# Kernel tuning notes

Hardware: AMD Instinct MI355X
Metric: run time of the kernel (lower is better)

Reference implementation:

```python
import jax, jax.numpy as jnp
import numpy as np

N_NUM = 100        # numerical columns
N_CAT = 100        # categorical columns
CAT_COUNT = 100    # categories per categorical column
N_COND = 128
EPS = 1e-5         # torch GroupNorm default eps


def setup_inputs() -> dict:
    key = jax.random.key(0)
    ks = jax.random.split(key, 8)
    B = 4096
    return {
        "x_num": jax.random.normal(ks[0], (B, N_NUM), dtype=jnp.float32),
        "x_cat": jax.random.randint(ks[1], (B, N_CAT), 0, CAT_COUNT),
        "W_num": jax.random.normal(ks[2], (N_NUM, N_COND), dtype=jnp.float32),
        "b_num": jax.random.normal(ks[3], (N_NUM, N_COND), dtype=jnp.float32),
        "emb_table": jax.random.normal(ks[4], (N_CAT * CAT_COUNT, N_COND), dtype=jnp.float32),
        "gn_w": jnp.ones((N_CAT, N_COND), dtype=jnp.float32),
        "gn_b": jnp.zeros((N_CAT, N_COND), dtype=jnp.float32),
        "W_cat": jax.random.normal(ks[5], (N_CAT, N_COND, N_COND), dtype=jnp.float32) / np.sqrt(N_COND).astype(np.float32),
        "b_cat": jax.random.normal(ks[6], (N_CAT, N_COND), dtype=jnp.float32),
    }


def reference(x_num, x_cat, W_num, b_num, emb_table, gn_w, gn_b, W_cat, b_cat):
    # --- numerical branch: grouped 1x1 conv (Cin/g=1, Cout/g=n_cond) + sigmoid ---
    # (B, n_num, 1) * (n_num, n_cond) + bias -> (B, n_num, n_cond)
    num_emb = jax.nn.sigmoid(x_num[:, :, None] * W_num[None] + b_num[None])

    # --- categorical branch ---
    offsets = jnp.arange(N_CAT, dtype=x_cat.dtype) * CAT_COUNT  # cat_offset
    emb = emb_table[x_cat + offsets[None]]  # (B, n_cat, n_cond)

    # GroupNorm with n_cat groups over n_cat*n_cond channels (spatial dim = 1):
    # normalize each column's n_cond features per sample (biased variance).
    mean = jnp.mean(emb, axis=-1, keepdims=True)
    var = jnp.var(emb, axis=-1, keepdims=True)
    normed = (emb - mean) * jax.lax.rsqrt(var + EPS)
    normed = normed * gn_w[None] + gn_b[None]

    # grouped 1x1 conv, groups = n_cat: per-column n_cond x n_cond matmul
    cat_emb = jax.nn.sigmoid(jnp.einsum('bgi,gio->bgo', normed, W_cat) + b_cat[None])

    M = jnp.concatenate([num_emb, cat_emb], axis=1)  # (B, n_num+n_cat, n_cond)
    return jnp.transpose(M, (0, 2, 1))               # (B, n_cond, n_num+n_cat)
```

## Files before the change

### kernel.cpp

```cpp
#include <hip/hip_runtime.h>
#include <cstdint>

#define NNUM 100
#define NCAT 100
#define CATC 100
#define NCOND 128
#define GN_EPS 1e-5f

typedef __attribute__((ext_vector_type(8))) short bfrag8;
typedef __attribute__((ext_vector_type(4))) float accf4;

__device__ __forceinline__ float sigmoidf_(float x) { return 1.0f / (1.0f + __expf(-x)); }

__device__ __forceinline__ ushort f2bf(float f) {
    uint32_t u = __builtin_bit_cast(uint32_t, f);
    u += 0x7fffu + ((u >> 16) & 1u);
    return (ushort)(u >> 16);
}
__device__ __forceinline__ float bf2f(ushort h) {
    return __builtin_bit_cast(float, (uint32_t)h << 16);
}

__global__ __launch_bounds__(256)
void prep_wcat(const float* __restrict__ W_cat, ushort* __restrict__ Wf)
{
    const int g    = blockIdx.x;
    const int lane = threadIdx.x & 63;
    const int w    = threadIdx.x >> 6;
    const float* Wg = W_cat + ((size_t)g << 14);
    ushort* Wfg = Wf + ((size_t)g << 15);
    #pragma unroll
    for (int i = 0; i < 8; ++i) {
        int p  = w * 8 + i;
        int t  = p >> 2, kk = p & 3;
        int c  = t * 16 + (lane & 15);
        int kb = kk * 32 + ((lane >> 4) << 3);
        ushort hi[8], lo[8];
        #pragma unroll
        for (int j = 0; j < 8; ++j) {
            float v = Wg[(kb + j) * NCOND + c];
            ushort h = f2bf(v);
            hi[j] = h;
            lo[j] = f2bf(v - bf2f(h));
        }
        int off = ((t * 4 + kk) * 2) * 512 + lane * 8;
        *(bfrag8*)(Wfg + off)       = *(const bfrag8*)hi;
        *(bfrag8*)(Wfg + off + 512) = *(const bfrag8*)lo;
    }
}

template<int DIRECT>
__global__ __launch_bounds__(256, 2)
void cat_gemm_kernel(const int* __restrict__ x_cat,
                     const float* __restrict__ emb_table,
                     const float* __restrict__ gn_w,
                     const float* __restrict__ gn_b,
                     const ushort* __restrict__ Wf,
                     const float* __restrict__ b_cat,
                     float* __restrict__ dst)
{
    const int g    = blockIdx.y;
    const int b0   = blockIdx.x * 128;
    const int tid  = threadIdx.x;
    const int lane = tid & 63;
    const int w    = tid >> 6;

    __shared__ __align__(16) ushort Ahi[128 * 128];
    __shared__ __align__(16) ushort Alo[128 * 128];

    const int half = lane >> 5;
    const int l5   = lane & 31;
    float4 gwv = *(const float4*)(gn_w + g * NCOND + l5 * 4);
    float4 gbv = *(const float4*)(gn_b + g * NCOND + l5 * 4);

    #pragma unroll 4
    for (int it = 0; it < 16; ++it) {
        int m = w * 32 + it * 2 + half;
        int b = b0 + m;
        int idx = x_cat[(size_t)b * NCAT + g];
        const float4* row = (const float4*)(emb_table + ((size_t)(g * CATC + idx) << 7));
        float4 v = row[l5];
        float s  = v.x + v.y + v.z + v.w;
        float ss = v.x * v.x + v.y * v.y + v.z * v.z + v.w * v.w;
        #pragma unroll
        for (int off = 16; off > 0; off >>= 1) {
            s  += __shfl_xor(s,  off, 64);
            ss += __shfl_xor(ss, off, 64);
        }
        float mean = s * 0.0078125f;
        float var  = fmaf(-mean, mean, ss * 0.0078125f);
        float rs   = rsqrtf(var + GN_EPS);
        float n0 = fmaf((v.x - mean) * rs, gwv.x, gbv.x);
        float n1 = fmaf((v.y - mean) * rs, gwv.y, gbv.y);
        float n2 = fmaf((v.z - mean) * rs, gwv.z, gbv.z);
        float n3 = fmaf((v.w - mean) * rs, gwv.w, gbv.w);
        ushort h0 = f2bf(n0), h1 = f2bf(n1), h2 = f2bf(n2), h3 = f2bf(n3);
        uint2 hp = { (uint32_t)h0 | ((uint32_t)h1 << 16),
                     (uint32_t)h2 | ((uint32_t)h3 << 16) };
        uint2 lp = { (uint32_t)f2bf(n0 - bf2f(h0)) | ((uint32_t)f2bf(n1 - bf2f(h1)) << 16),
                     (uint32_t)f2bf(n2 - bf2f(h2)) | ((uint32_t)f2bf(n3 - bf2f(h3)) << 16) };
        int bo = m * 256 + ((l5 * 8) ^ ((m & 7) << 4));
        *(uint2*)((char*)Ahi + bo) = hp;
        *(uint2*)((char*)Alo + bo) = lp;
    }
    __syncthreads();

    accf4 acc[2][8];
    #pragma unroll
    for (int gi = 0; gi < 2; ++gi)
        #pragma unroll
        for (int t = 0; t < 8; ++t)
            acc[gi][t] = (accf4){0.f, 0.f, 0.f, 0.f};

    const ushort* Wfg = Wf + ((size_t)g << 15);
    const int row0 = w * 16 + (lane & 15);
    const int sw   = (lane & 7) << 4;

    #pragma unroll
    for (int kk = 0; kk < 4; ++kk) {
        int colb = kk * 64 + ((lane >> 4) << 4);
        int o0 = row0 * 256 + (colb ^ sw);
        int o1 = o0 + 64 * 256;
        bfrag8 ah0 = *(const bfrag8*)((const char*)Ahi + o0);
        bfrag8 al0 = *(const bfrag8*)((const char*)Alo + o0);
        bfrag8 ah1 = *(const bfrag8*)((const char*)Ahi + o1);
        bfrag8 al1 = *(const bfrag8*)((const char*)Alo + o1);
        const ushort* wbase = Wfg + kk * 1024 + lane * 8;
        #pragma unroll
        for (int t = 0; t < 8; ++t) {
            bfrag8 wh = *(const bfrag8*)(wbase + t * 4096);
            bfrag8 wl = *(const bfrag8*)(wbase + t * 4096 + 512);
            acc[0][t] = __builtin_amdgcn_mfma_f32_16x16x32_bf16(ah0, wh, acc[0][t], 0, 0, 0);
            acc[0][t] = __builtin_amdgcn_mfma_f32_16x16x32_bf16(ah0, wl, acc[0][t], 0, 0, 0);
            acc[0][t] = __builtin_amdgcn_mfma_f32_16x16x32_bf16(al0, wh, acc[0][t], 0, 0, 0);
            acc[1][t] = __builtin_amdgcn_mfma_f32_16x16x32_bf16(ah1, wh, acc[1][t], 0, 0, 0);
            acc[1][t] = __builtin_amdgcn_mfma_f32_16x16x32_bf16(ah1, wl, acc[1][t], 0, 0, 0);
            acc[1][t] = __builtin_amdgcn_mfma_f32_16x16x32_bf16(al1, wh, acc[1][t], 0, 0, 0);
        }
    }

    const float* bcg = b_cat + g * NCOND;
    const int colL = lane & 15;
    const int quad = lane >> 4;
    #pragma unroll
    for (int t = 0; t < 8; ++t) {
        int c = t * 16 + colL;
        float bc = bcg[c];
        #pragma unroll
        for (int gi = 0; gi < 2; ++gi) {
            int mbase = (w + gi * 4) * 16 + quad * 4;
            #pragma unroll
            for (int r = 0; r < 4; ++r) {
                int b = b0 + mbase + r;
                float v = sigmoidf_(acc[gi][t][r] + bc);
                if (DIRECT) {
                    dst[(size_t)b * (128 * 200) + (size_t)c * 200 + 100 + g] = v;
                } else {
                    dst[(size_t)b * (NCAT * NCOND) + g * NCOND + c] = v;
                }
            }
        }
    }
}

__global__ __launch_bounds__(256)
void transpose_wn(const float* __restrict__ W_num, const float* __restrict__ b_num,
                  float* __restrict__ Wt, float* __restrict__ Bt)
{
    int idx = blockIdx.x * 256 + threadIdx.x;
    if (idx < NCOND * NNUM) {
        int c = idx / NNUM, j = idx - c * NNUM;
        Wt[idx] = W_num[j * NCOND + c];
        Bt[idx] = b_num[j * NCOND + c];
    }
}

__global__ __launch_bounds__(256)
void finalize_kernel(const float* __restrict__ ws_cat,
                     const float* __restrict__ Wt,
                     const float* __restrict__ Bt,
                     const float* __restrict__ x_num,
                     float* __restrict__ out)
{
    const int b   = blockIdx.x;
    const int tid = threadIdx.x;
    __shared__ float T[NCAT * 129];
    __shared__ float xr[NNUM];

    if (tid < NNUM) xr[tid] = x_num[b * NNUM + tid];

    const float4* src = (const float4*)(ws_cat + (size_t)b * (NCAT * NCOND));
    #pragma unroll
    for (int it = 0; it < 13; ++it) {
        int i4 = it * 256 + tid;
        if (i4 < (NCAT * NCOND) / 4) {
            float4 v = src[i4];
            int base = i4 * 4;
            int gg = base >> 7;
            int cc = base & 127;
            float* d = &T[gg * 129 + cc];
            d[0] = v.x; d[1] = v.y; d[2] = v.z; d[3] = v.w;
        }
    }
    __syncthreads();

    float4* outb = (float4*)(out + (size_t)b * (NCOND * 200));
    const float4* Wt4 = (const float4*)Wt;
    const float4* Bt4 = (const float4*)Bt;
    #pragma unroll
    for (int it = 0; it < 25; ++it) {
        int o4 = it * 256 + tid;
        int c  = o4 / 50;
        int j4 = o4 - c * 50;
        float4 v;
        if (j4 < 25) {
            float4 wv = Wt4[c * 25 + j4];
            float4 bv = Bt4[c * 25 + j4];
            int j = j4 * 4;
            v.x = sigmoidf_(fmaf(xr[j],     wv.x, bv.x));
            v.y = sigmoidf_(fmaf(xr[j + 1], wv.y, bv.y));
            v.z = sigmoidf_(fmaf(xr[j + 2], wv.z, bv.z));
            v.w = sigmoidf_(fmaf(xr[j + 3], wv.w, bv.w));
        } else {
            int gg = (j4 - 25) * 4;
            v.x = T[(gg    ) * 129 + c];
            v.y = T[(gg + 1) * 129 + c];
            v.z = T[(gg + 2) * 129 + c];
            v.w = T[(gg + 3) * 129 + c];
        }
        outb[o4] = v;
    }
}

__global__ __launch_bounds__(256)
void num_direct(const float* __restrict__ x_num, const float* __restrict__ W_num,
                const float* __restrict__ b_num, float* __restrict__ out, int B)
{
    size_t i = (size_t)blockIdx.x * 256 + threadIdx.x;
    size_t total = (size_t)B * NCOND * NNUM;
    if (i >= total) return;
    int n = (int)(i % NNUM);
    size_t t = i / NNUM;
    int c = (int)(t % NCOND);
    int b = (int)(t / NCOND);
    float v = sigmoidf_(x_num[b * NNUM + n] * W_num[n * NCOND + c] + b_num[n * NCOND + c]);
    out[(size_t)b * (NCOND * 200) + (size_t)c * 200 + n] = v;
}

extern "C" void kernel_launch(void* const* d_in, const int* in_sizes, int n_in,
                              void* d_out, int out_size, void* d_ws, size_t ws_size,
                              hipStream_t stream)
{
    const float* x_num  = (const float*)d_in[0];
    const int*   x_cat  = (const int*)  d_in[1];
    const float* W_num  = (const float*)d_in[2];
    const float* b_num  = (const float*)d_in[3];
    const float* emb    = (const float*)d_in[4];
    const float* gn_w   = (const float*)d_in[5];
    const float* gn_b   = (const float*)d_in[6];
    const float* W_cat  = (const float*)d_in[7];
    const float* b_cat  = (const float*)d_in[8];
    float* out = (float*)d_out;

    const int B = in_sizes[0] / NNUM;
    const size_t cat_bytes = (size_t)B * NCAT * NCOND * sizeof(float);
    const size_t need = cat_bytes + 2 * (size_t)NCOND * NNUM * sizeof(float);

    dim3 gemm_grid(B / 128, NCAT);

    if (ws_size >= need) {
        float* ws_cat = (float*)d_ws;
        float* Wt = (float*)((char*)d_ws + cat_bytes);
        float* Bt = Wt + NCOND * NNUM;
        ushort* Wf = (ushort*)out;
        prep_wcat<<<NCAT, 256, 0, stream>>>(W_cat, Wf);
        transpose_wn<<<(NCOND * NNUM + 255) / 256, 256, 0, stream>>>(W_num, b_num, Wt, Bt);
        cat_gemm_kernel<0><<<gemm_grid, 256, 0, stream>>>(x_cat, emb, gn_w, gn_b, Wf, b_cat, ws_cat);
        finalize_kernel<<<B, 256, 0, stream>>>(ws_cat, Wt, Bt, x_num, out);
    } else {
        ushort* Wf = (ushort*)d_ws;
        prep_wcat<<<NCAT, 256, 0, stream>>>(W_cat, Wf);
        cat_gemm_kernel<1><<<gemm_grid, 256, 0, stream>>>(x_cat, emb, gn_w, gn_b, Wf, b_cat, out);
        size_t total = (size_t)B * NCOND * NNUM;
        num_direct<<<(total + 255) / 256, 256, 0, stream>>>(x_num, W_num, b_num, out, B);
    }
}
```

Before: 622.9 us.

## Drop block barrier in cat GEMM, shuffle indices, split finalize across channel halves

The categorical GEMM now loads each wave's category indices once and broadcasts them with shuffles, instead of one global load per row. Each wave now consumes only the A rows it wrote itself, so the block-wide barrier is replaced by an LDS wait. The finalize kernel is split into two blocks per sample, one per half of the channels, which halves its shared memory and raises occupancy. The packed weights move into the workspace when there is room for them. Together these aim to cut gather latency, barrier stalls and finalize occupancy limits, at the cost of depending on per-wave data ownership to stay correct.

```diff
diff --git a/kernel.cpp b/kernel.cpp
--- a/kernel.cpp
+++ b/kernel.cpp
@@ -73,11 +73,13 @@
     float4 gwv = *(const float4*)(gn_w + g * NCOND + l5 * 4);
     float4 gbv = *(const float4*)(gn_b + g * NCOND + l5 * 4);
 
-    #pragma unroll 4
+    int myidx = x_cat[(size_t)(b0 + w * 32 + (lane & 31)) * NCAT + g];
+
+    #pragma unroll 8
     for (int it = 0; it < 16; ++it) {
-        int m = w * 32 + it * 2 + half;
-        int b = b0 + m;
-        int idx = x_cat[(size_t)b * NCAT + g];
+        int r = it * 2 + half;
+        int m = w * 32 + r;
+        int idx = __shfl(myidx, r, 64);
         const float4* row = (const float4*)(emb_table + ((size_t)(g * CATC + idx) << 7));
         float4 v = row[l5];
         float s  = v.x + v.y + v.z + v.w;
@@ -103,7 +105,7 @@
         *(uint2*)((char*)Ahi + bo) = hp;
         *(uint2*)((char*)Alo + bo) = lp;
     }
-    __syncthreads();
+    asm volatile("s_waitcnt lgkmcnt(0)" ::: "memory");
 
     accf4 acc[2][8];
     #pragma unroll
@@ -113,14 +115,14 @@
             acc[gi][t] = (accf4){0.f, 0.f, 0.f, 0.f};
 
     const ushort* Wfg = Wf + ((size_t)g << 15);
-    const int row0 = w * 16 + (lane & 15);
+    const int row0 = w * 32 + (lane & 15);
     const int sw   = (lane & 7) << 4;
 
     #pragma unroll
     for (int kk = 0; kk < 4; ++kk) {
         int colb = kk * 64 + ((lane >> 4) << 4);
         int o0 = row0 * 256 + (colb ^ sw);
-        int o1 = o0 + 64 * 256;
+        int o1 = o0 + 16 * 256;
         bfrag8 ah0 = *(const bfrag8*)((const char*)Ahi + o0);
         bfrag8 al0 = *(const bfrag8*)((const char*)Alo + o0);
         bfrag8 ah1 = *(const bfrag8*)((const char*)Ahi + o1);
@@ -148,7 +150,7 @@
         float bc = bcg[c];
         #pragma unroll
         for (int gi = 0; gi < 2; ++gi) {
-            int mbase = (w + gi * 4) * 16 + quad * 4;
+            int mbase = (2 * w + gi) * 16 + quad * 4;
             #pragma unroll
             for (int r = 0; r < 4; ++r) {
                 int b = b0 + mbase + r;
@@ -183,52 +185,55 @@
                      float* __restrict__ out)
 {
     const int b   = blockIdx.x;
+    const int h   = blockIdx.y;
     const int tid = threadIdx.x;
-    __shared__ float T[NCAT * 129];
+    __shared__ float T[NCAT * 65];
     __shared__ float xr[NNUM];
 
     if (tid < NNUM) xr[tid] = x_num[b * NNUM + tid];
 
     const float4* src = (const float4*)(ws_cat + (size_t)b * (NCAT * NCOND));
     #pragma unroll
-    for (int it = 0; it < 13; ++it) {
+    for (int it = 0; it < 7; ++it) {
         int i4 = it * 256 + tid;
-        if (i4 < (NCAT * NCOND) / 4) {
-            float4 v = src[i4];
-            int base = i4 * 4;
-            int gg = base >> 7;
-            int cc = base & 127;
-            float* d = &T[gg * 129 + cc];
+        if (i4 < NCAT * 16) {
+            int gg  = i4 >> 4;
+            int cc4 = i4 & 15;
+            float4 v = src[gg * 32 + h * 16 + cc4];
+            float* d = &T[gg * 65 + cc4 * 4];
             d[0] = v.x; d[1] = v.y; d[2] = v.z; d[3] = v.w;
         }
     }
     __syncthreads();
 
-    float4* outb = (float4*)(out + (size_t)b * (NCOND * 200));
+    float4* outb = (float4*)(out + (size_t)b * (NCOND * 200)) + h * 3200;
     const float4* Wt4 = (const float4*)Wt;
     const float4* Bt4 = (const float4*)Bt;
     #pragma unroll
-    for (int it = 0; it < 25; ++it) {
+    for (int it = 0; it < 13; ++it) {
         int o4 = it * 256 + tid;
-        int c  = o4 / 50;
-        int j4 = o4 - c * 50;
-        float4 v;
-        if (j4 < 25) {
-            float4 wv = Wt4[c * 25 + j4];
-            float4 bv = Bt4[c * 25 + j4];
-            int j = j4 * 4;
-            v.x = sigmoidf_(fmaf(xr[j],     wv.x, bv.x));
-            v.y = sigmoidf_(fmaf(xr[j + 1], wv.y, bv.y));
-            v.z = sigmoidf_(fmaf(xr[j + 2], wv.z, bv.z));
-            v.w = sigmoidf_(fmaf(xr[j + 3], wv.w, bv.w));
-        } else {
-            int gg = (j4 - 25) * 4;
-            v.x = T[(gg    ) * 129 + c];
-            v.y = T[(gg + 1) * 129 + c];
-            v.z = T[(gg + 2) * 129 + c];
-            v.w = T[(gg + 3) * 129 + c];
-        }
-        outb[o4] = v;
+        if (o4 < 64 * 50) {
+            int c_loc = o4 / 50;
+            int j4    = o4 - c_loc * 50;
+            int c     = h * 64 + c_loc;
+            float4 v;
+            if (j4 < 25) {
+                float4 wv = Wt4[c * 25 + j4];
+                float4 bv = Bt4[c * 25 + j4];
+                int j = j4 * 4;
+                v.x = sigmoidf_(fmaf(xr[j],     wv.x, bv.x));
+                v.y = sigmoidf_(fmaf(xr[j + 1], wv.y, bv.y));
+                v.z = sigmoidf_(fmaf(xr[j + 2], wv.z, bv.z));
+                v.w = sigmoidf_(fmaf(xr[j + 3], wv.w, bv.w));
+            } else {
+                int gg = (j4 - 25) * 4;
+                v.x = T[(gg    ) * 65 + c_loc];
+                v.y = T[(gg + 1) * 65 + c_loc];
+                v.z = T[(gg + 2) * 65 + c_loc];
+                v.w = T[(gg + 3) * 65 + c_loc];
+            }
+            outb[o4] = v;
+        }
     }
 }
 
@@ -264,7 +269,10 @@
 
     const int B = in_sizes[0] / NNUM;
     const size_t cat_bytes = (size_t)B * NCAT * NCOND * sizeof(float);
-    const size_t need = cat_bytes + 2 * (size_t)NCOND * NNUM * sizeof(float);
+    const size_t wtbt     = 2 * (size_t)NCOND * NNUM * sizeof(float);
+    const size_t wf_bytes = (size_t)NCAT * 32768 * sizeof(ushort);
+    const size_t need  = cat_bytes + wtbt;
+    const size_t need2 = need + wf_bytes;
 
     dim3 gemm_grid(B / 128, NCAT);
 
@@ -272,11 +280,12 @@
         float* ws_cat = (float*)d_ws;
         float* Wt = (float*)((char*)d_ws + cat_bytes);
         float* Bt = Wt + NCOND * NNUM;
-        ushort* Wf = (ushort*)out;
+        ushort* Wf = (ws_size >= need2) ? (ushort*)((char*)d_ws + need)
+                                        : (ushort*)out;
         prep_wcat<<<NCAT, 256, 0, stream>>>(W_cat, Wf);
         transpose_wn<<<(NCOND * NNUM + 255) / 256, 256, 0, stream>>>(W_num, b_num, Wt, Bt);
         cat_gemm_kernel<0><<<gemm_grid, 256, 0, stream>>>(x_cat, emb, gn_w, gn_b, Wf, b_cat, ws_cat);
-        finalize_kernel<<<B, 256, 0, stream>>>(ws_cat, Wt, Bt, x_num, out);
+        finalize_kernel<<<dim3(B, 2), 256, 0, stream>>>(ws_cat, Wt, Bt, x_num, out);
     } else {
         ushort* Wf = (ushort*)d_ws;
         prep_wcat<<<NCAT, 256, 0, stream>>>(W_cat, Wf);
```

Result: no change. 624.7 us (+0.3%).
